# Kernel tuning notes

Hardware: AMD Instinct MI355X
Metric: run time of the kernel (lower is better)

The kernel has to match this reference:

```python
import jax, jax.numpy as jnp
import numpy as np

B, T, C, H, MAX_LEN = 16, 512, 1024, 16, 512
D = C // H  # head_dim = 64

def setup_inputs() -> dict:
    key = jax.random.key(0)
    ks = jax.random.split(key, 10)
    s = 1.0 / np.sqrt(C)
    return {
        "x": jax.random.normal(ks[0], (B, T, C), dtype=jnp.float32),
        "Wq": jax.random.normal(ks[1], (C, C), dtype=jnp.float32) * s,
        "bq": jnp.zeros((C,), dtype=jnp.float32),
        "Wk": jax.random.normal(ks[2], (C, C), dtype=jnp.float32) * s,
        "bk": jnp.zeros((C,), dtype=jnp.float32),
        "Wv": jax.random.normal(ks[3], (C, C), dtype=jnp.float32) * s,
        "bv": jnp.zeros((C,), dtype=jnp.float32),
        "Wo": jax.random.normal(ks[4], (C, C), dtype=jnp.float32) * s,
        "bo": jnp.zeros((C,), dtype=jnp.float32),
        "rel_pos_bias": jax.random.normal(ks[5], (H, MAX_LEN, MAX_LEN), dtype=jnp.float32) * 0.02,
    }

def reference(x, Wq, bq, Wk, bk, Wv, bv, Wo, bo, rel_pos_bias):
    scale = 1.0 / jnp.sqrt(jnp.float32(D))
    # projections (torch Linear: x @ W.T + b), reshape to (B,H,T,D)
    def proj(W, b):
        return (x @ W.T + b).reshape(B, T, H, D).transpose(0, 2, 1, 3)
    q, k, v = proj(Wq, bq), proj(Wk, bk), proj(Wv, bv)
    attn = jnp.einsum('bhtd,bhsd->bhts', q, k) * scale  # (B,H,T,T)
    attn = attn + rel_pos_bias[None, :, :T, :T]
    causal = jnp.triu(jnp.ones((T, T), dtype=bool), k=1)
    attn = jnp.where(causal[None, None], -jnp.inf, attn)
    attn = jax.nn.softmax(attn, axis=-1)  # dropout p=0 (eval) -> identity
    out = jnp.einsum('bhts,bhsd->bhtd', attn, v)
    out = out.transpose(0, 2, 1, 3).reshape(B, T, C)
    return out @ Wo.T + bo
```

## Files before the change

### kernel.cpp

```cpp
#include <hip/hip_runtime.h>
#include <stdint.h>
#include <math.h>

#define DEV static __device__ __forceinline__

typedef __attribute__((ext_vector_type(8))) __bf16 bf16x8;
typedef __attribute__((ext_vector_type(4))) float f32x4;
typedef unsigned short u16;

DEV u16 f2b(float f) {
  union { float f; uint32_t u; } x; x.f = f;
  uint32_t r = x.u + 0x7fffu + ((x.u >> 16) & 1u);
  return (u16)(r >> 16);
}

DEV uint32_t pk2(float a, float b) {
  return (uint32_t)f2b(a) | ((uint32_t)f2b(b) << 16);
}

DEV float b2f_lo(uint32_t u) { return __uint_as_float(u << 16); }
DEV float b2f_hi(uint32_t u) { return __uint_as_float(u & 0xffff0000u); }

DEV void glds16(const void* g, void* l) {
  __builtin_amdgcn_global_load_lds(
      (const __attribute__((address_space(1))) void*)g,
      (__attribute__((address_space(3))) void*)l, 16, 0, 0);
}

DEV f32x4 mfma16(bf16x8 a, bf16x8 b, f32x4 c) {
  return __builtin_amdgcn_mfma_f32_16x16x32_bf16(a, b, c, 0, 0, 0);
}

__global__ __launch_bounds__(256) void cvt_all(
    const float* __restrict__ x, const float* __restrict__ Wq,
    const float* __restrict__ Wk, const float* __restrict__ Wv,
    const float* __restrict__ Wo, const float* __restrict__ bias,
    u16* __restrict__ xb, u16* __restrict__ wqkv, u16* __restrict__ wo,
    u16* __restrict__ biasb) {
  size_t i = ((size_t)blockIdx.x * 256 + threadIdx.x) * 4;
  const float* s;
  u16* d;
  size_t off;
  float scale = 1.0f;
  if (i < 8388608)        { s = x;  d = xb;             off = i; }
  else if (i < 9437184)   { s = Wq; d = wqkv;           off = i - 8388608; }
  else if (i < 10485760)  { s = Wk; d = wqkv + 1048576; off = i - 9437184; }
  else if (i < 11534336)  { s = Wv; d = wqkv + 2097152; off = i - 10485760; }
  else if (i < 12582912)  { s = Wo; d = wo;             off = i - 11534336; }
  else { s = bias; d = biasb; off = i - 12582912; scale = 1.44269504f; }
  float4 v = *(const float4*)(s + off);
  ushort4 o;
  o.x = f2b(v.x * scale); o.y = f2b(v.y * scale);
  o.z = f2b(v.z * scale); o.w = f2b(v.w * scale);
  *(ushort4*)(d + off) = o;
}

__global__ __launch_bounds__(256) void gemm_qkv(
    const u16* __restrict__ A, const u16* __restrict__ Bw,
    const float* __restrict__ bq, const float* __restrict__ bk,
    const float* __restrict__ bv,
    u16* __restrict__ qo, u16* __restrict__ ko, u16* __restrict__ vto) {
  __shared__ u16 lsA[2][128 * 32];
  __shared__ u16 lsB[2][128 * 32];
  const int K = 1024;
  int tid = threadIdx.x, wave = tid >> 6, lane = tid & 63;
  int q16 = lane >> 4, c16 = lane & 15;
  int m0 = blockIdx.y * 128, n0 = blockIdx.x * 128;
  int wm = wave >> 1, wn = wave & 1;
  const bool vblk = (n0 >= 2048);
  const u16* lsR = vblk ? &lsB[0][0] : &lsA[0][0];
  const u16* lsC = vblk ? &lsA[0][0] : &lsB[0][0];
  int wr = vblk ? wn : wm;
  int wc = vblk ? wm : wn;

  f32x4 acc[4][4];
#pragma unroll
  for (int i = 0; i < 4; ++i)
#pragma unroll
    for (int j = 0; j < 4; ++j) acc[i][j] = (f32x4)0.0f;

  int srow = (lane >> 2);
  int scol = ((lane & 3) ^ ((lane >> 3) & 3)) * 8;
  int swz = (q16 ^ ((c16 >> 1) & 3)) * 8;

  for (int k0 = 0; k0 < K; k0 += 64) {
    __syncthreads();
#pragma unroll
    for (int half = 0; half < 2; ++half) {
#pragma unroll
      for (int cc = 0; cc < 2; ++cc) {
        int chunk = wave * 2 + cc;
        int r = chunk * 16 + srow;
        glds16(A + (size_t)(m0 + r) * K + k0 + half * 32 + scol,
               &lsA[half][chunk * 512]);
        glds16(Bw + (size_t)(n0 + r) * K + k0 + half * 32 + scol,
               &lsB[half][chunk * 512]);
      }
    }
    __syncthreads();
#pragma unroll
    for (int half = 0; half < 2; ++half) {
      bf16x8 rf[4], cf[4];
#pragma unroll
      for (int i = 0; i < 4; ++i)
        rf[i] = *(const bf16x8*)&lsR[half * 4096 +
                                     (wr * 64 + i * 16 + c16) * 32 + swz];
#pragma unroll
      for (int i = 0; i < 4; ++i)
        cf[i] = *(const bf16x8*)&lsC[half * 4096 +
                                     (wc * 64 + i * 16 + c16) * 32 + swz];
#pragma unroll
      for (int it = 0; it < 4; ++it)
#pragma unroll
        for (int jt = 0; jt < 4; ++jt)
          acc[it][jt] = mfma16(rf[it], cf[jt], acc[it][jt]);
    }
  }

  if (!vblk) {
#pragma unroll
    for (int mt = 0; mt < 4; ++mt) {
#pragma unroll
      for (int nt = 0; nt < 4; ++nt) {
        int n = n0 + wn * 64 + nt * 16 + c16;
        int which = n >> 10;
        int nl = n & 1023;
        int hh = nl >> 6, d = nl & 63;
        float bias = (which == 0 ? bq : bk)[nl];
        u16* dst = (which == 0 ? qo : ko);
#pragma unroll
        for (int r = 0; r < 4; ++r) {
          int m = m0 + wm * 64 + mt * 16 + q16 * 4 + r;
          int b = m >> 9, t = m & 511;
          size_t bh = (size_t)b * 16 + hh;
          dst[(bh * 512 + t) * 72 + d] = f2b(acc[mt][nt][r] + bias);
        }
      }
    }
  } else {
#pragma unroll
    for (int it = 0; it < 4; ++it) {
      int nbase = n0 + wn * 64 + it * 16 + q16 * 4;
      float4 bvv = *(const float4*)(bv + (nbase & 1023));
#pragma unroll
      for (int jt = 0; jt < 4; ++jt) {
        int m = m0 + wm * 64 + jt * 16 + c16;
        int b = m >> 9, t = m & 511;
        size_t bh4 = ((size_t)b * 16) * 4;
#pragma unroll
        for (int r = 0; r < 4; ++r) {
          int nl = (nbase + r) & 1023;
          int hh = nl >> 6, d = nl & 63;
          float bias = ((const float*)&bvv)[r];
          vto[((bh4 + (size_t)hh * 4 + (t >> 7)) * 64 + d) * 136 + (t & 127)] =
              f2b(acc[it][jt][r] + bias);
        }
      }
    }
  }
}

__global__ __launch_bounds__(256, 3) void attn_kernel(
    const u16* __restrict__ qglob, const u16* __restrict__ kglob,
    const u16* __restrict__ vtglob, const u16* __restrict__ biasb,
    u16* __restrict__ og) {
  __shared__ u16 lsK[128 * 72];
  __shared__ u16 lsV[64 * 136];
  __shared__ u16 lsP[4 * 32 * 72];

  int tid = threadIdx.x, wave = tid >> 6, lane = tid & 63;
  int q16 = lane >> 4, c16 = lane & 15;
  u16* lsPw = lsP + wave * (32 * 72);

  int p = blockIdx.x;
  int bx, bh, bx2 = -1, bh2 = 0;
  if (p < 256)      { bx = 3; bh = p; }
  else if (p < 512) { bx = 2; bh = p - 256; bx2 = 0; bh2 = p - 256; }
  else              { int q = p - 512; bx = 1; bh = 2 * q; bx2 = 1; bh2 = 2 * q + 1; }

  for (;;) {
    int b = bh >> 4, h = bh & 15;
    int q0 = bx * 128;

    const u16* qbase = qglob + (size_t)bh * (512 * 72) + (size_t)q0 * 72;
    const u16* kbase = kglob + (size_t)bh * (512 * 72);
    const u16* vbase = vtglob + (size_t)bh * 4 * (64 * 136);

    for (int i = wave; i < 18; i += 4)
      glds16(qbase + (size_t)i * 512 + lane * 8, lsK + i * 512);
    __syncthreads();
    bf16x8 qf[2][2];
#pragma unroll
    for (int nt = 0; nt < 2; ++nt)
#pragma unroll
      for (int ks = 0; ks < 2; ++ks)
        qf[nt][ks] = *(const bf16x8*)&lsK[(wave * 32 + nt * 16 + c16) * 72 +
                                          ks * 32 + q16 * 8];

    f32x4 oacc[2][4];
#pragma unroll
    for (int i = 0; i < 2; ++i)
#pragma unroll
      for (int j = 0; j < 4; ++j) oacc[i][j] = (f32x4)0.0f;
    float mold[2] = {-INFINITY, -INFINITY};
    float lsum[2] = {0.0f, 0.0f};
    const float SCL = 0.18033688f;

    for (int st = 0; st <= bx; ++st) {
      bool diag = (st == bx);
      __syncthreads();
      const u16* kt = kbase + (size_t)st * (128 * 72);
      for (int i = wave; i < 18; i += 4)
        glds16(kt + (size_t)i * 512 + lane * 8, lsK + i * 512);
      const u16* vt = vbase + (size_t)st * (64 * 136);
      for (int i = wave; i < 17; i += 4)
        glds16(vt + (size_t)i * 512 + lane * 8, lsV + i * 512);

      uint2 ub[2][8];
#pragma unroll
      for (int nt = 0; nt < 2; ++nt) {
        int qgl = q0 + wave * 32 + nt * 16 + c16;
        const u16* bp =
            biasb + ((size_t)h * 512 + qgl) * 512 + st * 128 + q16 * 4;
#pragma unroll
        for (int mt = 0; mt < 8; ++mt) ub[nt][mt] = *(const uint2*)(bp + mt * 16);
      }
      __syncthreads();

      f32x4 sa[8][2];
#pragma unroll
      for (int mt = 0; mt < 8; ++mt) {
        sa[mt][0] = (f32x4)0.0f;
        sa[mt][1] = (f32x4)0.0f;
      }
      int mtmax = diag ? 2 * wave + 2 : 8;
#pragma unroll
      for (int mt = 0; mt < 8; ++mt) {
        if (mt < mtmax) {
#pragma unroll
          for (int ks = 0; ks < 2; ++ks) {
            bf16x8 kf =
                *(const bf16x8*)&lsK[(mt * 16 + c16) * 72 + ks * 32 + q16 * 8];
            sa[mt][0] = mfma16(kf, qf[0][ks], sa[mt][0]);
            sa[mt][1] = mfma16(kf, qf[1][ks], sa[mt][1]);
          }
        }
      }

      float alpha[2];
#pragma unroll
      for (int nt = 0; nt < 2; ++nt) {
#pragma unroll
        for (int mt = 0; mt < 8; ++mt) {
          uint32_t lo = ub[nt][mt].x, hi = ub[nt][mt].y;
          f32x4 bv;
          bv[0] = b2f_lo(lo); bv[1] = b2f_hi(lo);
          bv[2] = b2f_lo(hi); bv[3] = b2f_hi(hi);
          sa[mt][nt] = sa[mt][nt] * SCL + bv;
        }
        if (diag) {
#pragma unroll
          for (int mt = 0; mt < 8; ++mt) {
            int d0 = mt * 16 + q16 * 4 - wave * 32 - nt * 16 - c16;
#pragma unroll
            for (int r = 0; r < 4; ++r)
              if (d0 + r > 0) sa[mt][nt][r] = -INFINITY;
          }
        }
        f32x4 m4 = sa[0][nt];
#pragma unroll
        for (int mt = 1; mt < 8; ++mt) {
          f32x4 v = sa[mt][nt];
          m4[0] = fmaxf(m4[0], v[0]); m4[1] = fmaxf(m4[1], v[1]);
          m4[2] = fmaxf(m4[2], v[2]); m4[3] = fmaxf(m4[3], v[3]);
        }
        float mx = fmaxf(fmaxf(m4[0], m4[1]), fmaxf(m4[2], m4[3]));
        mx = fmaxf(mx, __shfl_xor(mx, 16));
        mx = fmaxf(mx, __shfl_xor(mx, 32));
        float mnew = fmaxf(mold[nt], mx);
        alpha[nt] = exp2f(mold[nt] - mnew);
        mold[nt] = mnew;
        f32x4 s4 = (f32x4)0.0f;
#pragma unroll
        for (int mt = 0; mt < 8; ++mt) {
          f32x4 pq;
          pq[0] = exp2f(sa[mt][nt][0] - mnew);
          pq[1] = exp2f(sa[mt][nt][1] - mnew);
          pq[2] = exp2f(sa[mt][nt][2] - mnew);
          pq[3] = exp2f(sa[mt][nt][3] - mnew);
          sa[mt][nt] = pq;
          s4 += pq;
        }
        float ss = (s4[0] + s4[1]) + (s4[2] + s4[3]);
        ss += __shfl_xor(ss, 16);
        ss += __shfl_xor(ss, 32);
        lsum[nt] = lsum[nt] * alpha[nt] + ss;
      }

#pragma unroll
      for (int mo = 0; mo < 2; ++mo) {
        f32x4 av;
#pragma unroll
        for (int r = 0; r < 4; ++r) av[r] = __shfl(alpha[mo], q16 * 4 + r);
#pragma unroll
        for (int dt = 0; dt < 4; ++dt) oacc[mo][dt] *= av;
      }

      int G = diag ? wave + 1 : 4;
#pragma unroll
      for (int hf = 0; hf < 2; ++hf) {
        if (hf * 2 < G) {
#pragma unroll
          for (int nt = 0; nt < 2; ++nt)
#pragma unroll
            for (int mt4 = 0; mt4 < 4; ++mt4) {
              f32x4 pv = sa[hf * 4 + mt4][nt];
              uint2 w;
              w.x = pk2(pv[0], pv[1]);
              w.y = pk2(pv[2], pv[3]);
              *(uint2*)&lsPw[(nt * 16 + c16) * 72 + mt4 * 16 + q16 * 4] = w;
            }
#pragma unroll
          for (int ksh = 0; ksh < 2; ++ksh) {
            if (hf * 2 + ksh < G) {
              bf16x8 pf0 =
                  *(const bf16x8*)&lsPw[c16 * 72 + ksh * 32 + q16 * 8];
              bf16x8 pf1 =
                  *(const bf16x8*)&lsPw[(16 + c16) * 72 + ksh * 32 + q16 * 8];
#pragma unroll
              for (int dt = 0; dt < 4; ++dt) {
                bf16x8 vf = *(const bf16x8*)&lsV[(dt * 16 + c16) * 136 +
                                                 hf * 64 + ksh * 32 + q16 * 8];
                oacc[0][dt] = mfma16(pf0, vf, oacc[0][dt]);
                oacc[1][dt] = mfma16(pf1, vf, oacc[1][dt]);
              }
            }
          }
        }
      }
    }

#pragma unroll
    for (int mo = 0; mo < 2; ++mo) {
      f32x4 lv;
#pragma unroll
      for (int r = 0; r < 4; ++r) lv[r] = __shfl(lsum[mo], q16 * 4 + r);
#pragma unroll
      for (int r = 0; r < 4; ++r) {
        int tg = q0 + wave * 32 + mo * 16 + q16 * 4 + r;
        float inv = 1.0f / lv[r];
#pragma unroll
        for (int dt = 0; dt < 4; ++dt)
          og[((size_t)b * 512 + tg) * 1024 + h * 64 + dt * 16 + c16] =
              f2b(oacc[mo][dt][r] * inv);
      }
    }

    if (bx2 < 0) break;
    __syncthreads();
    bx = bx2; bh = bh2; bx2 = -1;
  }
}

__global__ __launch_bounds__(256) void gemm_out(
    const u16* __restrict__ A, const u16* __restrict__ W,
    const float* __restrict__ bo, float* __restrict__ out) {
  __shared__ u16 lsA[2][128 * 32];
  __shared__ u16 lsB[2][128 * 32];
  const int K = 1024;
  int tid = threadIdx.x, wave = tid >> 6, lane = tid & 63;
  int q16 = lane >> 4, c16 = lane & 15;
  int m0 = blockIdx.y * 128, n0 = blockIdx.x * 128;
  int wm = wave >> 1, wn = wave & 1;

  f32x4 acc[4][4];
#pragma unroll
  for (int i = 0; i < 4; ++i)
#pragma unroll
    for (int j = 0; j < 4; ++j) acc[i][j] = (f32x4)0.0f;

  int srow = (lane >> 2);
  int scol = ((lane & 3) ^ ((lane >> 3) & 3)) * 8;
  int swz = (q16 ^ ((c16 >> 1) & 3)) * 8;

  for (int k0 = 0; k0 < K; k0 += 64) {
    __syncthreads();
#pragma unroll
    for (int half = 0; half < 2; ++half) {
#pragma unroll
      for (int cc = 0; cc < 2; ++cc) {
        int chunk = wave * 2 + cc;
        int r = chunk * 16 + srow;
        glds16(A + (size_t)(m0 + r) * K + k0 + half * 32 + scol,
               &lsA[half][chunk * 512]);
        glds16(W + (size_t)(n0 + r) * K + k0 + half * 32 + scol,
               &lsB[half][chunk * 512]);
      }
    }
    __syncthreads();
#pragma unroll
    for (int half = 0; half < 2; ++half) {
      bf16x8 af[4], bf[4];
#pragma unroll
      for (int i = 0; i < 4; ++i)
        af[i] = *(const bf16x8*)&lsA[half][(wm * 64 + i * 16 + c16) * 32 + swz];
#pragma unroll
      for (int i = 0; i < 4; ++i)
        bf[i] = *(const bf16x8*)&lsB[half][(wn * 64 + i * 16 + c16) * 32 + swz];
#pragma unroll
      for (int mt = 0; mt < 4; ++mt)
#pragma unroll
        for (int nt = 0; nt < 4; ++nt)
          acc[mt][nt] = mfma16(af[mt], bf[nt], acc[mt][nt]);
    }
  }

#pragma unroll
  for (int mt = 0; mt < 4; ++mt) {
#pragma unroll
    for (int nt = 0; nt < 4; ++nt) {
      int n = n0 + wn * 64 + nt * 16 + c16;
      float bias = bo[n];
#pragma unroll
      for (int r = 0; r < 4; ++r) {
        int m = m0 + wm * 64 + mt * 16 + q16 * 4 + r;
        out[(size_t)m * 1024 + n] = acc[mt][nt][r] + bias;
      }
    }
  }
}

extern "C" void kernel_launch(void* const* d_in, const int* in_sizes, int n_in,
                              void* d_out, int out_size, void* d_ws, size_t ws_size,
                              hipStream_t stream) {
  const float* x    = (const float*)d_in[0];
  const float* Wq   = (const float*)d_in[1];
  const float* bq   = (const float*)d_in[2];
  const float* Wk   = (const float*)d_in[3];
  const float* bk   = (const float*)d_in[4];
  const float* Wv   = (const float*)d_in[5];
  const float* bv   = (const float*)d_in[6];
  const float* Wo   = (const float*)d_in[7];
  const float* bo   = (const float*)d_in[8];
  const float* bias = (const float*)d_in[9];
  float* out = (float*)d_out;

  const size_t MB = 1u << 20;
  char* ws = (char*)d_ws;
  u16* xb    = (u16*)(ws);
  u16* wqkv  = (u16*)(ws + 16 * MB);
  u16* wo    = (u16*)(ws + 22 * MB);
  u16* biasb = (u16*)(ws + 24 * MB);
  u16* qb    = (u16*)(ws + 32 * MB);
  u16* kb    = (u16*)(ws + 50 * MB);
  u16* vtb   = (u16*)(ws + 68 * MB);
  u16* ab    = xb;

  cvt_all<<<16384, 256, 0, stream>>>(x, Wq, Wk, Wv, Wo, bias,
                                     xb, wqkv, wo, biasb);
  gemm_qkv<<<dim3(24, 64), 256, 0, stream>>>(xb, wqkv, bq, bk, bv, qb, kb, vtb);
  attn_kernel<<<dim3(640), 256, 0, stream>>>(qb, kb, vtb, biasb, ab);
  gemm_out<<<dim3(8, 64), 256, 0, stream>>>(ab, wo, bo, out);
}
```

Measured before the change: 280.1 us.

## Use 256x128 tiles with an eight-wave, interleaved global-to-LDS pipelined GEMM core

The QKV and output projection GEMMs now share one core that runs 512-thread blocks on 256x128 tiles. LDS is double-buffered across k-tiles, and the next tile's global-to-LDS loads are interleaved with the MFMA phases, gated by explicit vmcnt/lgkmcnt waits, barriers and setprio. This is meant to hide global load latency behind matrix math and to raise reuse per block. The cost is 96KB of LDS per block, which may limit each CU to one block. The hand-counted vmcnt scheme is also fragile.

Result: slower. 286.8 us (+2.4%).

```diff
diff --git a/kernel.cpp b/kernel.cpp
--- a/kernel.cpp
+++ b/kernel.cpp
@@ -30,6 +30,15 @@
 DEV f32x4 mfma16(bf16x8 a, bf16x8 b, f32x4 c) {
   return __builtin_amdgcn_mfma_f32_16x16x32_bf16(a, b, c, 0, 0, 0);
 }
+
+#define BAR() __builtin_amdgcn_s_barrier()
+#define WAIT_LGKM()                                      \
+  {                                                      \
+    asm volatile("s_waitcnt lgkmcnt(0)" ::: "memory");   \
+    __builtin_amdgcn_sched_barrier(0);                   \
+  }
+#define WAIT_VM4() asm volatile("s_waitcnt vmcnt(4)" ::: "memory")
+#define WAIT_VM0() asm volatile("s_waitcnt vmcnt(0)" ::: "memory")
 
 __global__ __launch_bounds__(256) void cvt_all(
     const float* __restrict__ x, const float* __restrict__ Wq,
@@ -55,23 +64,133 @@
   *(ushort4*)(d + off) = o;
 }
 
-__global__ __launch_bounds__(256) void gemm_qkv(
+
+DEV void stage_a(const u16* A, int m0, int kt, int kh, int wave, int srow,
+                 int scol, u16 (*lsA)[2][8192]) {
+  const u16* src =
+      A + (size_t)(m0 + wave * 32 + srow) * 1024 + kt * 64 + kh * 32 + scol;
+  glds16(src, &lsA[kt & 1][kh][wave * 1024]);
+  glds16(src + (size_t)16 * 1024, &lsA[kt & 1][kh][wave * 1024 + 512]);
+}
+
+DEV void stage_b(const u16* Bw, int n0, int kt, int kh, int wave, int srow,
+                 int scol, u16 (*lsB)[2][4096]) {
+  glds16(Bw + (size_t)(n0 + wave * 16 + srow) * 1024 + kt * 64 + kh * 32 + scol,
+         &lsB[kt & 1][kh][wave * 512]);
+}
+
+DEV void load_frags(const u16* Rbase, const u16* Cbase, int wr, int wc,
+                    int c16, int swz, bf16x8 rf[4], bf16x8 cf[4]) {
+#pragma unroll
+  for (int i = 0; i < 4; ++i)
+    rf[i] = *(const bf16x8*)&Rbase[(wr * 64 + i * 16 + c16) * 32 + swz];
+#pragma unroll
+  for (int i = 0; i < 4; ++i)
+    cf[i] = *(const bf16x8*)&Cbase[(wc * 64 + i * 16 + c16) * 32 + swz];
+}
+
+template <int ILO>
+DEV void mfma_half(bf16x8 rf[4], bf16x8 cf[4], f32x4 acc[4][4]) {
+  __builtin_amdgcn_s_setprio(1);
+#pragma unroll
+  for (int j = 0; j < 4; ++j) acc[ILO][j] = mfma16(rf[ILO], cf[j], acc[ILO][j]);
+#pragma unroll
+  for (int j = 0; j < 4; ++j)
+    acc[ILO + 1][j] = mfma16(rf[ILO + 1], cf[j], acc[ILO + 1][j]);
+  __builtin_amdgcn_s_setprio(0);
+}
+
+DEV void gemm_core(const u16* A, const u16* Bw, int m0, int n0, bool vblk,
+                   int wave, int lane, u16 (*lsA)[2][8192],
+                   u16 (*lsB)[2][4096], f32x4 acc[4][4]) {
+  int q16 = lane >> 4, c16 = lane & 15;
+  int wm = wave >> 1, wn = wave & 1;
+  int wr = vblk ? wn : wm, wc = vblk ? wm : wn;
+  int srow = lane >> 2;
+  int scol = ((lane & 3) ^ ((lane >> 3) & 3)) * 8;
+  int swz = (q16 ^ ((c16 >> 1) & 3)) * 8;
+
+  stage_a(A, m0, 0, 0, wave, srow, scol, lsA);
+  stage_a(A, m0, 0, 1, wave, srow, scol, lsA);
+  stage_b(Bw, n0, 0, 0, wave, srow, scol, lsB);
+  stage_b(Bw, n0, 0, 1, wave, srow, scol, lsB);
+  stage_a(A, m0, 1, 0, wave, srow, scol, lsA);
+  stage_a(A, m0, 1, 1, wave, srow, scol, lsA);
+  WAIT_VM4();
+  BAR();
+
+  bf16x8 rf0[4], rf1[4], cf0[4], cf1[4];
+  for (int j = 0; j < 8; ++j) {
+    int t = 2 * j;
+    const u16* R00 = vblk ? &lsB[0][0][0] : &lsA[0][0][0];
+    const u16* C00 = vblk ? &lsA[0][0][0] : &lsB[0][0][0];
+    const u16* R01 = vblk ? &lsB[0][1][0] : &lsA[0][1][0];
+    const u16* C01 = vblk ? &lsA[0][1][0] : &lsB[0][1][0];
+    const u16* R10 = vblk ? &lsB[1][0][0] : &lsA[1][0][0];
+    const u16* C10 = vblk ? &lsA[1][0][0] : &lsB[1][0][0];
+    const u16* R11 = vblk ? &lsB[1][1][0] : &lsA[1][1][0];
+    const u16* C11 = vblk ? &lsA[1][1][0] : &lsB[1][1][0];
+    load_frags(R00, C00, wr, wc, c16, swz, rf0, cf0);
+    stage_b(Bw, n0, t + 1, 0, wave, srow, scol, lsB);
+    BAR();
+    WAIT_LGKM();
+    mfma_half<0>(rf0, cf0, acc);
+    BAR();
+    load_frags(R01, C01, wr, wc, c16, swz, rf1, cf1);
+    stage_b(Bw, n0, t + 1, 1, wave, srow, scol, lsB);
+    BAR();
+    WAIT_LGKM();
+    mfma_half<2>(rf0, cf0, acc);
+    BAR();
+    if (j < 7) stage_a(A, m0, t + 2, 0, wave, srow, scol, lsA);
+    BAR();
+    WAIT_LGKM();
+    mfma_half<0>(rf1, cf1, acc);
+    BAR();
+    if (j < 7) stage_a(A, m0, t + 2, 1, wave, srow, scol, lsA);
+    BAR();
+    WAIT_LGKM();
+    mfma_half<2>(rf1, cf1, acc);
+    if (j < 7) { WAIT_VM4(); } else { WAIT_VM0(); }
+    BAR();
+    load_frags(R10, C10, wr, wc, c16, swz, rf0, cf0);
+    if (j < 7) stage_b(Bw, n0, t + 2, 0, wave, srow, scol, lsB);
+    BAR();
+    WAIT_LGKM();
+    mfma_half<0>(rf0, cf0, acc);
+    BAR();
+    load_frags(R11, C11, wr, wc, c16, swz, rf1, cf1);
+    if (j < 7) stage_b(Bw, n0, t + 2, 1, wave, srow, scol, lsB);
+    BAR();
+    WAIT_LGKM();
+    mfma_half<2>(rf0, cf0, acc);
+    BAR();
+    if (j < 7) stage_a(A, m0, t + 3, 0, wave, srow, scol, lsA);
+    BAR();
+    WAIT_LGKM();
+    mfma_half<0>(rf1, cf1, acc);
+    BAR();
+    if (j < 7) stage_a(A, m0, t + 3, 1, wave, srow, scol, lsA);
+    BAR();
+    WAIT_LGKM();
+    mfma_half<2>(rf1, cf1, acc);
+    if (j < 7) { WAIT_VM4(); } else { WAIT_VM0(); }
+    BAR();
+  }
+}
+
+__global__ __launch_bounds__(512, 2) void gemm_qkv(
     const u16* __restrict__ A, const u16* __restrict__ Bw,
     const float* __restrict__ bq, const float* __restrict__ bk,
     const float* __restrict__ bv,
     u16* __restrict__ qo, u16* __restrict__ ko, u16* __restrict__ vto) {
-  __shared__ u16 lsA[2][128 * 32];
-  __shared__ u16 lsB[2][128 * 32];
-  const int K = 1024;
+  __shared__ u16 lsA[2][2][8192];
+  __shared__ u16 lsB[2][2][4096];
   int tid = threadIdx.x, wave = tid >> 6, lane = tid & 63;
   int q16 = lane >> 4, c16 = lane & 15;
-  int m0 = blockIdx.y * 128, n0 = blockIdx.x * 128;
+  int m0 = blockIdx.y * 256, n0 = blockIdx.x * 128;
   int wm = wave >> 1, wn = wave & 1;
   const bool vblk = (n0 >= 2048);
-  const u16* lsR = vblk ? &lsB[0][0] : &lsA[0][0];
-  const u16* lsC = vblk ? &lsA[0][0] : &lsB[0][0];
-  int wr = vblk ? wn : wm;
-  int wc = vblk ? wm : wn;
 
   f32x4 acc[4][4];
 #pragma unroll
@@ -79,43 +198,7 @@
 #pragma unroll
     for (int j = 0; j < 4; ++j) acc[i][j] = (f32x4)0.0f;
 
-  int srow = (lane >> 2);
-  int scol = ((lane & 3) ^ ((lane >> 3) & 3)) * 8;
-  int swz = (q16 ^ ((c16 >> 1) & 3)) * 8;
-
-  for (int k0 = 0; k0 < K; k0 += 64) {
-    __syncthreads();
-#pragma unroll
-    for (int half = 0; half < 2; ++half) {
-#pragma unroll
-      for (int cc = 0; cc < 2; ++cc) {
-        int chunk = wave * 2 + cc;
-        int r = chunk * 16 + srow;
-        glds16(A + (size_t)(m0 + r) * K + k0 + half * 32 + scol,
-               &lsA[half][chunk * 512]);
-        glds16(Bw + (size_t)(n0 + r) * K + k0 + half * 32 + scol,
-               &lsB[half][chunk * 512]);
-      }
-    }
-    __syncthreads();
-#pragma unroll
-    for (int half = 0; half < 2; ++half) {
-      bf16x8 rf[4], cf[4];
-#pragma unroll
-      for (int i = 0; i < 4; ++i)
-        rf[i] = *(const bf16x8*)&lsR[half * 4096 +
-                                     (wr * 64 + i * 16 + c16) * 32 + swz];
-#pragma unroll
-      for (int i = 0; i < 4; ++i)
-        cf[i] = *(const bf16x8*)&lsC[half * 4096 +
-                                     (wc * 64 + i * 16 + c16) * 32 + swz];
-#pragma unroll
-      for (int it = 0; it < 4; ++it)
-#pragma unroll
-        for (int jt = 0; jt < 4; ++jt)
-          acc[it][jt] = mfma16(rf[it], cf[jt], acc[it][jt]);
-    }
-  }
+  gemm_core(A, Bw, m0, n0, vblk, wave, lane, lsA, lsB, acc);
 
   if (!vblk) {
 #pragma unroll
@@ -362,15 +445,14 @@
   }
 }
 
-__global__ __launch_bounds__(256) void gemm_out(
+__global__ __launch_bounds__(512, 2) void gemm_out(
     const u16* __restrict__ A, const u16* __restrict__ W,
     const float* __restrict__ bo, float* __restrict__ out) {
-  __shared__ u16 lsA[2][128 * 32];
-  __shared__ u16 lsB[2][128 * 32];
-  const int K = 1024;
+  __shared__ u16 lsA[2][2][8192];
+  __shared__ u16 lsB[2][2][4096];
   int tid = threadIdx.x, wave = tid >> 6, lane = tid & 63;
   int q16 = lane >> 4, c16 = lane & 15;
-  int m0 = blockIdx.y * 128, n0 = blockIdx.x * 128;
+  int m0 = blockIdx.y * 256, n0 = blockIdx.x * 128;
   int wm = wave >> 1, wn = wave & 1;
 
   f32x4 acc[4][4];
@@ -379,41 +461,7 @@
 #pragma unroll
     for (int j = 0; j < 4; ++j) acc[i][j] = (f32x4)0.0f;
 
-  int srow = (lane >> 2);
-  int scol = ((lane & 3) ^ ((lane >> 3) & 3)) * 8;
-  int swz = (q16 ^ ((c16 >> 1) & 3)) * 8;
-
-  for (int k0 = 0; k0 < K; k0 += 64) {
-    __syncthreads();
-#pragma unroll
-    for (int half = 0; half < 2; ++half) {
-#pragma unroll
-      for (int cc = 0; cc < 2; ++cc) {
-        int chunk = wave * 2 + cc;
-        int r = chunk * 16 + srow;
-        glds16(A + (size_t)(m0 + r) * K + k0 + half * 32 + scol,
-               &lsA[half][chunk * 512]);
-        glds16(W + (size_t)(n0 + r) * K + k0 + half * 32 + scol,
-               &lsB[half][chunk * 512]);
-      }
-    }
-    __syncthreads();
-#pragma unroll
-    for (int half = 0; half < 2; ++half) {
-      bf16x8 af[4], bf[4];
-#pragma unroll
-      for (int i = 0; i < 4; ++i)
-        af[i] = *(const bf16x8*)&lsA[half][(wm * 64 + i * 16 + c16) * 32 + swz];
-#pragma unroll
-      for (int i = 0; i < 4; ++i)
-        bf[i] = *(const bf16x8*)&lsB[half][(wn * 64 + i * 16 + c16) * 32 + swz];
-#pragma unroll
-      for (int mt = 0; mt < 4; ++mt)
-#pragma unroll
-        for (int nt = 0; nt < 4; ++nt)
-          acc[mt][nt] = mfma16(af[mt], bf[nt], acc[mt][nt]);
-    }
-  }
+  gemm_core(A, W, m0, n0, false, wave, lane, lsA, lsB, acc);
 
 #pragma unroll
   for (int mt = 0; mt < 4; ++mt) {
@@ -458,7 +506,7 @@
 
   cvt_all<<<16384, 256, 0, stream>>>(x, Wq, Wk, Wv, Wo, bias,
                                      xb, wqkv, wo, biasb);
-  gemm_qkv<<<dim3(24, 64), 256, 0, stream>>>(xb, wqkv, bq, bk, bv, qb, kb, vtb);
+  gemm_qkv<<<dim3(24, 32), 512, 0, stream>>>(xb, wqkv, bq, bk, bv, qb, kb, vtb);
   attn_kernel<<<dim3(640), 256, 0, stream>>>(qb, kb, vtb, biasb, ab);
-  gemm_out<<<dim3(8, 64), 256, 0, stream>>>(ab, wo, bo, out);
-}
+  gemm_out<<<dim3(8, 32), 512, 0, stream>>>(ab, wo, bo, out);
+}
```
